# Kernel optimization log

Measured on AMD Instinct MI355X. Metric: run time of the kernel, lower is better.

Reference implementation:

```python
import jax, jax.numpy as jnp
import numpy as np

B, T, D_IN, D_OUT = 4, 2048, 1024, 1024

def setup_inputs() -> dict:
    key = jax.random.key(0)
    k0, k1, k2, k3 = jax.random.split(key, 4)
    s = 1.0 / np.sqrt(D_IN)
    return {
        "x": jax.random.normal(k0, (B, T, D_IN), dtype=jnp.float32),
        "w_query": jax.random.normal(k1, (D_OUT, D_IN), dtype=jnp.float32) * s,
        "w_key": jax.random.normal(k2, (D_OUT, D_IN), dtype=jnp.float32) * s,
        "w_value": jax.random.normal(k3, (D_OUT, D_IN), dtype=jnp.float32) * s,
    }

def reference(x, w_query, w_key, w_value):
    # Linear (no bias): y = x @ W.T, W has shape (d_out, d_in)
    q = jnp.einsum('btd,od->bto', x, w_query)   # (B,T,d_out)
    k = jnp.einsum('btd,od->bto', x, w_key)
    v = jnp.einsum('btd,od->bto', x, w_value)
    scale = 1.0 / jnp.sqrt(jnp.asarray(k.shape[-1], dtype=x.dtype))
    scores = jnp.einsum('bqo,bko->bqk', q, k) * scale  # (B,T,T)
    t = scores.shape[-1]
    causal = jnp.tril(jnp.ones((t, t), dtype=bool))    # True = keep
    scores = jnp.where(causal, scores, -jnp.inf)
    weights = jax.nn.softmax(scores, axis=-1)
    # dropout rate is 0.0 -> identity
    context = jnp.einsum('bqk,bko->bqo', weights, v)   # (B,T,d_out)
    return context
```

## Files before the change

kernel.cpp:

```cpp
#include <hip/hip_runtime.h>
#include <hip/hip_bf16.h>

#define NB 4
#define TT 2048
#define DD 1024
#define MM (NB*TT)

using f32x4  = __attribute__((ext_vector_type(4))) float;
using bf16x8 = __attribute__((ext_vector_type(8))) __bf16;
using u16x8  = __attribute__((ext_vector_type(8))) unsigned short;

__device__ __forceinline__ unsigned short f2b(float f) {
  __hip_bfloat16 h = __float2bfloat16(f);
  return *reinterpret_cast<unsigned short*>(&h);
}

__device__ __forceinline__ float b2f(unsigned short u) {
  __hip_bfloat16 h = *reinterpret_cast<__hip_bfloat16*>(&u);
  return __bfloat162float(h);
}

__device__ __forceinline__ void gld_lds16(const void* g, void* l) {
  __builtin_amdgcn_global_load_lds(
      (const __attribute__((address_space(1))) void*)g,
      (__attribute__((address_space(3))) void*)l, 16, 0, 0);
}

__device__ __forceinline__ void bar() {
  asm volatile("" ::: "memory");
  __builtin_amdgcn_s_barrier();
  asm volatile("" ::: "memory");
}

__global__ void k_cvt4(const float* __restrict__ x,  const float* __restrict__ wq,
                       const float* __restrict__ wk, const float* __restrict__ wv,
                       unsigned short* __restrict__ xb, unsigned short* __restrict__ wqb,
                       unsigned short* __restrict__ wkb, unsigned short* __restrict__ wvb) {
  const int nx = MM*DD/4, nw = DD*DD/4;
  const int ntot = nx + 3*nw;
  int i = blockIdx.x * blockDim.x + threadIdx.x;
  int stride = gridDim.x * blockDim.x;
  for (; i < ntot; i += stride) {
    const float* s; unsigned short* d; int j;
    if (i < nx)            { s = x;  d = xb;  j = i; }
    else if (i < nx + nw)  { s = wq; d = wqb; j = i - nx; }
    else if (i < nx + 2*nw){ s = wk; d = wkb; j = i - nx - nw; }
    else                   { s = wv; d = wvb; j = i - nx - 2*nw; }
    float4 v = reinterpret_cast<const float4*>(s)[j];
    ushort4 o;
    o.x = f2b(v.x); o.y = f2b(v.y); o.z = f2b(v.z); o.w = f2b(v.w);
    reinterpret_cast<ushort4*>(d)[j] = o;
  }
}

__launch_bounds__(512, 2)
__global__ void k_qkv8(const unsigned short* __restrict__ xb,
                       const unsigned short* __restrict__ wqb,
                       const unsigned short* __restrict__ wkb,
                       const unsigned short* __restrict__ wvb,
                       unsigned short* __restrict__ Qb,
                       unsigned short* __restrict__ Kb,
                       unsigned short* __restrict__ Vt) {
  __shared__ __align__(16) char Lds[131072];
  const int tid = threadIdx.x;
  const int l = tid & 63, wid = tid >> 6;
  const int l15 = l & 15, l4 = l >> 4;
  const int wm = wid >> 2, wn = wid & 3;
  const int z = blockIdx.z;
  const unsigned short* W = (z == 0) ? wqb : (z == 1) ? wkb : wvb;
  const size_t m0 = (size_t)blockIdx.x * 256;
  const size_t n0 = (size_t)blockIdx.y * 256;

  int srow[2], scb[2];
  #pragma unroll
  for (int j = 0; j < 2; ++j) {
    int d  = (j*512 + tid) * 16;
    int sd = d ^ (((d >> 7) & 7) << 4);
    srow[j] = sd >> 7;
    scb[j]  = sd & 127;
  }
  const char* pA[2][2]; const char* pB[2][2];
  #pragma unroll
  for (int h = 0; h < 2; ++h)
    #pragma unroll
    for (int j = 0; j < 2; ++j) {
      pA[h][j] = (const char*)xb + ((m0 + h*128 + srow[j]) * DD) * 2 + scb[j];
      pB[h][j] = (const char*)W  + ((n0 + h*128 + srow[j]) * DD) * 2 + scb[j];
    }
  char* ldsA = Lds;
  char* ldsB = Lds + 65536;

#define STG(p, ldsr, slot, half, kt) do {                                         \
    gld_lds16(p[half][0] + (size_t)(kt)*128,                                      \
              (ldsr) + (slot)*32768 + (half)*16384 + wid*1024);                   \
    gld_lds16(p[half][1] + (size_t)(kt)*128,                                      \
              (ldsr) + (slot)*32768 + (half)*16384 + 8192 + wid*1024);            \
  } while (0)

#define SWZ(x) ((x) ^ ((((x) >> 7) & 7) << 4))
#define KTQ 16
  STG(pA, ldsA, 0, 0, 0);
  STG(pA, ldsA, 0, 1, 0);
  STG(pB, ldsB, 0, 0, 0);
  STG(pB, ldsB, 0, 1, 0);
  STG(pA, ldsA, 1, 0, 1);
  STG(pA, ldsA, 1, 1, 1);
  STG(pB, ldsB, 1, 0, 1);
  asm volatile("s_waitcnt vmcnt(6)" ::: "memory");
  bar();

  f32x4 acc[8][4] = {};
  bf16x8 afL[4][2], afU[4][2], bfL[2][2], bfR[2][2];

#define TILE(t, S) do {                                                           \
    const int tn = ((t)+1 < KTQ) ? (t)+1 : 0;                                     \
    const int t2 = ((t)+2 < KTQ) ? (t)+2 : 0;                                     \
           \
    _Pragma("unroll") for (int m = 0; m < 4; ++m)                                 \
      _Pragma("unroll") for (int kk = 0; kk < 2; ++kk) {                          \
        int lg = m*2048 + l15*128 + kk*64 + l4*16;                                \
        afL[m][kk] = *(const bf16x8*)(ldsA + (S)*32768 + wm*16384 + SWZ(lg)); }   \
    _Pragma("unroll") for (int n = 0; n < 2; ++n)                                 \
      _Pragma("unroll") for (int kk = 0; kk < 2; ++kk) {                          \
        int lg = ((wn&1)*64 + n*16 + l15)*128 + kk*64 + l4*16;                    \
        bfL[n][kk] = *(const bf16x8*)(ldsB + (S)*32768 + (wn>>1)*16384 + SWZ(lg)); } \
    STG(pB, ldsB, (S)^1, 1, tn);                                                  \
    bar();                                                                        \
    asm volatile("s_waitcnt lgkmcnt(0)" ::: "memory");                            \
    __builtin_amdgcn_sched_barrier(0);                                            \
    __builtin_amdgcn_s_setprio(1);                                                \
    _Pragma("unroll") for (int m = 0; m < 4; ++m)                                 \
      _Pragma("unroll") for (int n = 0; n < 2; ++n)                               \
        _Pragma("unroll") for (int kk = 0; kk < 2; ++kk)                          \
          acc[m][n] = __builtin_amdgcn_mfma_f32_16x16x32_bf16(afL[m][kk], bfL[n][kk], acc[m][n], 0,0,0); \
    __builtin_amdgcn_s_setprio(0);                                                \
    bar();                                                                        \
                                    \
    _Pragma("unroll") for (int m = 0; m < 4; ++m)                                 \
      _Pragma("unroll") for (int kk = 0; kk < 2; ++kk) {                          \
        int lg = (m+4)*2048 + l15*128 + kk*64 + l4*16;                            \
        afU[m][kk] = *(const bf16x8*)(ldsA + (S)*32768 + wm*16384 + SWZ(lg)); }   \
    bar();                                                                        \
    asm volatile("s_waitcnt lgkmcnt(0)" ::: "memory");                            \
    __builtin_amdgcn_sched_barrier(0);                                            \
    __builtin_amdgcn_s_setprio(1);                                                \
    _Pragma("unroll") for (int m = 0; m < 4; ++m)                                 \
      _Pragma("unroll") for (int n = 0; n < 2; ++n)                               \
        _Pragma("unroll") for (int kk = 0; kk < 2; ++kk)                          \
          acc[m+4][n] = __builtin_amdgcn_mfma_f32_16x16x32_bf16(afU[m][kk], bfL[n][kk], acc[m+4][n], 0,0,0); \
    __builtin_amdgcn_s_setprio(0);                                                \
    bar();                                                                        \
                    \
    _Pragma("unroll") for (int n = 0; n < 2; ++n)                                 \
      _Pragma("unroll") for (int kk = 0; kk < 2; ++kk) {                          \
        int lg = ((wn&1)*64 + (n+2)*16 + l15)*128 + kk*64 + l4*16;                \
        bfR[n][kk] = *(const bf16x8*)(ldsB + (S)*32768 + (wn>>1)*16384 + SWZ(lg)); } \
    STG(pA, ldsA, S, 0, t2);                                                      \
    bar();                                                                        \
    asm volatile("s_waitcnt lgkmcnt(0)" ::: "memory");                            \
    __builtin_amdgcn_sched_barrier(0);                                            \
    __builtin_amdgcn_s_setprio(1);                                                \
    _Pragma("unroll") for (int m = 0; m < 4; ++m)                                 \
      _Pragma("unroll") for (int n = 0; n < 2; ++n)                               \
        _Pragma("unroll") for (int kk = 0; kk < 2; ++kk)                          \
          acc[m+4][n+2] = __builtin_amdgcn_mfma_f32_16x16x32_bf16(afU[m][kk], bfR[n][kk], acc[m+4][n+2], 0,0,0); \
    __builtin_amdgcn_s_setprio(0);                                                \
    bar();                                                                        \
              \
    STG(pA, ldsA, S, 1, t2);                                                      \
    STG(pB, ldsB, S, 0, t2);                                                      \
    asm volatile("s_waitcnt vmcnt(6)" ::: "memory");                              \
    bar();                                                                        \
    __builtin_amdgcn_s_setprio(1);                                                \
    _Pragma("unroll") for (int m = 0; m < 4; ++m)                                 \
      _Pragma("unroll") for (int n = 0; n < 2; ++n)                               \
        _Pragma("unroll") for (int kk = 0; kk < 2; ++kk)                          \
          acc[m][n+2] = __builtin_amdgcn_mfma_f32_16x16x32_bf16(afL[m][kk], bfR[n][kk], acc[m][n+2], 0,0,0); \
    __builtin_amdgcn_s_setprio(0);                                                \
    bar();                                                                        \
  } while (0)

  for (int tp = 0; tp < KTQ; tp += 2) {
    TILE(tp, 0);
    TILE(tp + 1, 1);
  }
#undef TILE
#undef STG
#undef SWZ
  asm volatile("s_waitcnt vmcnt(0)" ::: "memory");

  if (z < 2) {
    unsigned short* out = (z == 0) ? Qb : Kb;
    #pragma unroll
    for (int m = 0; m < 8; ++m)
      #pragma unroll
      for (int n = 0; n < 4; ++n)
        #pragma unroll
        for (int r = 0; r < 4; ++r) {
          size_t row = m0 + wm*128 + m*16 + l4*4 + r;
          size_t col = n0 + wn*64  + n*16 + l15;
          out[row * DD + col] = f2b(acc[m][n][r]);
        }
  } else {
    #pragma unroll
    for (int m = 0; m < 8; ++m)
      #pragma unroll
      for (int n = 0; n < 4; ++n)
        #pragma unroll
        for (int r = 0; r < 4; ++r) {
          size_t row = m0 + wm*128 + m*16 + l4*4 + r;
          size_t col = n0 + wn*64  + n*16 + l15;
          size_t b = row >> 11, t = row & (TT - 1);
          Vt[(b * DD + col) * TT + t] = f2b(acc[m][n][r]);
        }
  }
}

__launch_bounds__(256)
__global__ void k_scores(const unsigned short* __restrict__ Qb,
                         const unsigned short* __restrict__ Kb,
                         unsigned short* __restrict__ S) {
  __shared__ __align__(16) unsigned short As[128*32];
  __shared__ __align__(16) unsigned short Bs[128*32];
  const int tid = threadIdx.x;
  const int l = tid & 63, wid = tid >> 6;
  const int l15 = l & 15, l4 = l >> 4;
  const int wr = (wid >> 1) * 64, wc = (wid & 1) * 64;

  const int b = blockIdx.x / 136;
  int t = blockIdx.x % 136;
  int qi = 0;
  while ((qi + 1) * (qi + 2) / 2 <= t) qi++;
  const int ki = t - qi * (qi + 1) / 2;

  const size_t arow0 = (size_t)b * TT + qi * 128;
  const size_t brow0 = (size_t)b * TT + ki * 128;

  const int lrow = tid >> 2;
  const int lcol = (tid & 3) * 8;
  const unsigned short* Ap = Qb + (arow0 + lrow) * DD + lcol;
  const unsigned short* Bp = Kb + (brow0 + lrow) * DD + lcol;
  unsigned short* AsW = &As[wid * 512];
  unsigned short* BsW = &Bs[wid * 512];

  f32x4 acc[4][4] = {};

  for (int k0 = 0; k0 < DD; k0 += 32) {
    __syncthreads();
    gld_lds16(Ap + k0,           AsW);
    gld_lds16(Ap + 64*DD + k0,   AsW + 2048);
    gld_lds16(Bp + k0,           BsW);
    gld_lds16(Bp + 64*DD + k0,   BsW + 2048);
    __syncthreads();
    bf16x8 af[4], bfr[4];
    #pragma unroll
    for (int mi = 0; mi < 4; ++mi)
      af[mi] = *reinterpret_cast<const bf16x8*>(&As[(wr + mi*16 + l15)*32 + l4*8]);
    #pragma unroll
    for (int ni = 0; ni < 4; ++ni)
      bfr[ni] = *reinterpret_cast<const bf16x8*>(&Bs[(wc + ni*16 + l15)*32 + l4*8]);
    #pragma unroll
    for (int mi = 0; mi < 4; ++mi)
      #pragma unroll
      for (int ni = 0; ni < 4; ++ni)
        acc[mi][ni] = __builtin_amdgcn_mfma_f32_16x16x32_bf16(af[mi], bfr[ni], acc[mi][ni], 0, 0, 0);
  }

  const float scale = 0.03125f;
  #pragma unroll
  for (int mi = 0; mi < 4; ++mi)
    #pragma unroll
    for (int ni = 0; ni < 4; ++ni)
      #pragma unroll
      for (int r = 0; r < 4; ++r) {
        int row = wr + mi*16 + l4*4 + r;
        int col = wc + ni*16 + l15;
        int gq = qi*128 + row, gk = ki*128 + col;
        float v = (gk > gq) ? -1e30f : acc[mi][ni][r] * scale;
        S[((size_t)b * TT + gq) * TT + gk] = f2b(v);
      }
}

__launch_bounds__(256)
__global__ void k_softmax(unsigned short* __restrict__ S, float* __restrict__ rl) {
  const int tid = threadIdx.x;
  const int w = tid >> 6, l = tid & 63;
  const int row = blockIdx.x * 4 + w;
  const int b = row >> 11, q = row & (TT - 1);
  unsigned short* Srow = S + ((size_t)b * TT + q) * TT;
  const int width = ((q >> 7) + 1) << 7;

  float v[4][8];
  bool has[4];
  float mx = -1e30f;
  #pragma unroll
  for (int c = 0; c < 4; ++c) {
    const int off = c * 512 + l * 8;
    has[c] = off < width;
    if (has[c]) {
      u16x8 u = *reinterpret_cast<const u16x8*>(&Srow[off]);
      #pragma unroll
      for (int j = 0; j < 8; ++j) { v[c][j] = b2f(u[j]); mx = fmaxf(mx, v[c][j]); }
    }
  }
  #pragma unroll
  for (int mm = 1; mm < 64; mm <<= 1) mx = fmaxf(mx, __shfl_xor(mx, mm));

  float s = 0.f;
  #pragma unroll
  for (int c = 0; c < 4; ++c) {
    if (has[c]) {
      u16x8 u;
      #pragma unroll
      for (int j = 0; j < 8; ++j) {
        float p = __expf(v[c][j] - mx);
        s += p;
        u[j] = f2b(p);
      }
      *reinterpret_cast<u16x8*>(&Srow[c * 512 + l * 8]) = u;
    }
  }
  #pragma unroll
  for (int mm = 1; mm < 64; mm <<= 1) s += __shfl_xor(s, mm);
  if (l == 0) rl[row] = 1.0f / s;
}

__launch_bounds__(256)
__global__ void k_pv(const unsigned short* __restrict__ P,
                     const unsigned short* __restrict__ Vt,
                     const float* __restrict__ rl,
                     float* __restrict__ O) {
  __shared__ __align__(16) unsigned short As[128*32];
  __shared__ __align__(16) unsigned short Bs[128*32];
  const int tid = threadIdx.x;
  const int l = tid & 63, wid = tid >> 6;
  const int l15 = l & 15, l4 = l >> 4;
  const int wr = (wid >> 1) * 64, wc = (wid & 1) * 64;

  const int qi = 15 - (blockIdx.x >> 5);
  const int di = (blockIdx.x >> 2) & 7;
  const int b  = blockIdx.x & 3;
  const int KEXT = (qi + 1) * 128;

  const int lrow = tid >> 2;
  const int lcol = (tid & 3) * 8;
  const unsigned short* Ap = P  + ((size_t)b * TT + qi * 128 + lrow) * TT + lcol;
  const unsigned short* Bp = Vt + ((size_t)b * DD + di * 128 + lrow) * TT + lcol;
  unsigned short* AsW = &As[wid * 512];
  unsigned short* BsW = &Bs[wid * 512];

  f32x4 acc[4][4] = {};

  for (int k0 = 0; k0 < KEXT; k0 += 32) {
    __syncthreads();
    gld_lds16(Ap + k0,           AsW);
    gld_lds16(Ap + 64*TT + k0,   AsW + 2048);
    gld_lds16(Bp + k0,           BsW);
    gld_lds16(Bp + 64*TT + k0,   BsW + 2048);
    __syncthreads();
    bf16x8 af[4], bfr[4];
    #pragma unroll
    for (int mi = 0; mi < 4; ++mi)
      af[mi] = *reinterpret_cast<const bf16x8*>(&As[(wr + mi*16 + l15)*32 + l4*8]);
    #pragma unroll
    for (int ni = 0; ni < 4; ++ni)
      bfr[ni] = *reinterpret_cast<const bf16x8*>(&Bs[(wc + ni*16 + l15)*32 + l4*8]);
    #pragma unroll
    for (int mi = 0; mi < 4; ++mi)
      #pragma unroll
      for (int ni = 0; ni < 4; ++ni)
        acc[mi][ni] = __builtin_amdgcn_mfma_f32_16x16x32_bf16(af[mi], bfr[ni], acc[mi][ni], 0, 0, 0);
  }

  #pragma unroll
  for (int mi = 0; mi < 4; ++mi)
    #pragma unroll
    for (int ni = 0; ni < 4; ++ni)
      #pragma unroll
      for (int r = 0; r < 4; ++r) {
        int row = wr + mi*16 + l4*4 + r;
        int col = wc + ni*16 + l15;
        size_t q = (size_t)qi * 128 + row;
        O[((size_t)b * TT + q) * DD + di * 128 + col] =
            acc[mi][ni][r] * rl[(size_t)b * TT + q];
      }
}

extern "C" void kernel_launch(void* const* d_in, const int* in_sizes, int n_in,
                              void* d_out, int out_size, void* d_ws, size_t ws_size,
                              hipStream_t stream) {
  const float* x  = (const float*)d_in[0];
  const float* wq = (const float*)d_in[1];
  const float* wk = (const float*)d_in[2];
  const float* wv = (const float*)d_in[3];
  unsigned short* ws  = (unsigned short*)d_ws;
  unsigned short* Qb  = ws;
  unsigned short* Kb  = Qb + (size_t)MM * DD;
  unsigned short* Vt  = Kb + (size_t)MM * DD;
  unsigned short* Sb  = Vt + (size_t)MM * DD;
  unsigned short* xb  = Sb;
  unsigned short* wqb = xb + (size_t)MM * DD;
  unsigned short* wkb = wqb + (size_t)DD * DD;
  unsigned short* wvb = wkb + (size_t)DD * DD;
  float* rl = (float*)(Sb + (size_t)NB * TT * TT);
  float* out = (float*)d_out;

  k_cvt4<<<2048, 256, 0, stream>>>(x, wq, wk, wv, xb, wqb, wkb, wvb);
  k_qkv8<<<dim3(32, 4, 3), 512, 0, stream>>>(xb, wqb, wkb, wvb, Qb, Kb, Vt);
  k_scores<<<544, 256, 0, stream>>>(Qb, Kb, Sb);
  k_softmax<<<MM/4, 256, 0, stream>>>(Sb, rl);
  k_pv<<<512, 256, 0, stream>>>(Sb, Vt, rl, out);
}
```

Measured before the change: 188.5 us.

## Double K-step to 64 with XOR-swizzled LDS in scores and PV kernels

In the scores and PV GEMM kernels, the K step per iteration doubles from 32 to 64, so each barrier pair covers twice as much MFMA work. Global-to-LDS loads use an XOR-swizzled column mapping that matches a swizzled LDS read pattern, meant to avoid LDS bank conflicts with the wider 128-byte rows. The scores kernel also remaps block indices so concurrently scheduled blocks spread across batches and tiles. LDS use per block doubles, and the projection kernel edits are only reformatting of index arithmetic.

```diff
diff --git a/kernel.cpp b/kernel.cpp
--- a/kernel.cpp
+++ b/kernel.cpp
@@ -115,14 +115,14 @@
 #define TILE(t, S) do {                                                           \
     const int tn = ((t)+1 < KTQ) ? (t)+1 : 0;                                     \
     const int t2 = ((t)+2 < KTQ) ? (t)+2 : 0;                                     \
-           \
+      \
     _Pragma("unroll") for (int m = 0; m < 4; ++m)                                 \
       _Pragma("unroll") for (int kk = 0; kk < 2; ++kk) {                          \
-        int lg = m*2048 + l15*128 + kk*64 + l4*16;                                \
+        int lg = (m*16 + l15)*128 + (kk*64 + l4*16);                              \
         afL[m][kk] = *(const bf16x8*)(ldsA + (S)*32768 + wm*16384 + SWZ(lg)); }   \
     _Pragma("unroll") for (int n = 0; n < 2; ++n)                                 \
       _Pragma("unroll") for (int kk = 0; kk < 2; ++kk) {                          \
-        int lg = ((wn&1)*64 + n*16 + l15)*128 + kk*64 + l4*16;                    \
+        int lg = ((wn&1)*64 + n*16 + l15)*128 + (kk*64 + l4*16);                  \
         bfL[n][kk] = *(const bf16x8*)(ldsB + (S)*32768 + (wn>>1)*16384 + SWZ(lg)); } \
     STG(pB, ldsB, (S)^1, 1, tn);                                                  \
     bar();                                                                        \
@@ -135,10 +135,10 @@
           acc[m][n] = __builtin_amdgcn_mfma_f32_16x16x32_bf16(afL[m][kk], bfL[n][kk], acc[m][n], 0,0,0); \
     __builtin_amdgcn_s_setprio(0);                                                \
     bar();                                                                        \
-                                    \
+                        \
     _Pragma("unroll") for (int m = 0; m < 4; ++m)                                 \
       _Pragma("unroll") for (int kk = 0; kk < 2; ++kk) {                          \
-        int lg = (m+4)*2048 + l15*128 + kk*64 + l4*16;                            \
+        int lg = ((m+4)*16 + l15)*128 + (kk*64 + l4*16);                          \
         afU[m][kk] = *(const bf16x8*)(ldsA + (S)*32768 + wm*16384 + SWZ(lg)); }   \
     bar();                                                                        \
     asm volatile("s_waitcnt lgkmcnt(0)" ::: "memory");                            \
@@ -150,10 +150,10 @@
           acc[m+4][n] = __builtin_amdgcn_mfma_f32_16x16x32_bf16(afU[m][kk], bfL[n][kk], acc[m+4][n], 0,0,0); \
     __builtin_amdgcn_s_setprio(0);                                                \
     bar();                                                                        \
-                    \
+               \
     _Pragma("unroll") for (int n = 0; n < 2; ++n)                                 \
       _Pragma("unroll") for (int kk = 0; kk < 2; ++kk) {                          \
-        int lg = ((wn&1)*64 + (n+2)*16 + l15)*128 + kk*64 + l4*16;                \
+        int lg = ((wn&1)*64 + (n+2)*16 + l15)*128 + (kk*64 + l4*16);              \
         bfR[n][kk] = *(const bf16x8*)(ldsB + (S)*32768 + (wn>>1)*16384 + SWZ(lg)); } \
     STG(pA, ldsA, S, 0, t2);                                                      \
     bar();                                                                        \
@@ -166,7 +166,7 @@
           acc[m+4][n+2] = __builtin_amdgcn_mfma_f32_16x16x32_bf16(afU[m][kk], bfR[n][kk], acc[m+4][n+2], 0,0,0); \
     __builtin_amdgcn_s_setprio(0);                                                \
     bar();                                                                        \
-              \
+        \
     STG(pA, ldsA, S, 1, t2);                                                      \
     STG(pB, ldsB, S, 0, t2);                                                      \
     asm volatile("s_waitcnt vmcnt(6)" ::: "memory");                              \
@@ -220,15 +220,17 @@
 __global__ void k_scores(const unsigned short* __restrict__ Qb,
                          const unsigned short* __restrict__ Kb,
                          unsigned short* __restrict__ S) {
-  __shared__ __align__(16) unsigned short As[128*32];
-  __shared__ __align__(16) unsigned short Bs[128*32];
+  __shared__ __align__(16) unsigned short As[128*64];
+  __shared__ __align__(16) unsigned short Bs[128*64];
   const int tid = threadIdx.x;
   const int l = tid & 63, wid = tid >> 6;
   const int l15 = l & 15, l4 = l >> 4;
   const int wr = (wid >> 1) * 64, wc = (wid & 1) * 64;
 
-  const int b = blockIdx.x / 136;
-  int t = blockIdx.x % 136;
+  const int bid = blockIdx.x;
+  const int swz = (bid & 7) * 68 + (bid >> 3);
+  const int b = swz / 136;
+  int t = swz % 136;
   int qi = 0;
   while ((qi + 1) * (qi + 2) / 2 <= t) qi++;
   const int ki = t - qi * (qi + 1) / 2;
@@ -236,34 +238,44 @@
   const size_t arow0 = (size_t)b * TT + qi * 128;
   const size_t brow0 = (size_t)b * TT + ki * 128;
 
-  const int lrow = tid >> 2;
-  const int lcol = (tid & 3) * 8;
-  const unsigned short* Ap = Qb + (arow0 + lrow) * DD + lcol;
-  const unsigned short* Bp = Kb + (brow0 + lrow) * DD + lcol;
+  const int srow = wid * 8 + (l >> 3);
+  const int scol = 8 * ((l & 7) ^ (l >> 3));
+  const unsigned short* Ap = Qb + (arow0 + srow) * DD + scol;
+  const unsigned short* Bp = Kb + (brow0 + srow) * DD + scol;
   unsigned short* AsW = &As[wid * 512];
   unsigned short* BsW = &Bs[wid * 512];
 
   f32x4 acc[4][4] = {};
 
-  for (int k0 = 0; k0 < DD; k0 += 32) {
+  for (int k0 = 0; k0 < DD; k0 += 64) {
     __syncthreads();
-    gld_lds16(Ap + k0,           AsW);
-    gld_lds16(Ap + 64*DD + k0,   AsW + 2048);
-    gld_lds16(Bp + k0,           BsW);
-    gld_lds16(Bp + 64*DD + k0,   BsW + 2048);
+    #pragma unroll
+    for (int u = 0; u < 4; ++u) {
+      gld_lds16(Ap + (size_t)u*32*DD + k0, AsW + u*2048);
+      gld_lds16(Bp + (size_t)u*32*DD + k0, BsW + u*2048);
+    }
     __syncthreads();
-    bf16x8 af[4], bfr[4];
-    #pragma unroll
-    for (int mi = 0; mi < 4; ++mi)
-      af[mi] = *reinterpret_cast<const bf16x8*>(&As[(wr + mi*16 + l15)*32 + l4*8]);
-    #pragma unroll
-    for (int ni = 0; ni < 4; ++ni)
-      bfr[ni] = *reinterpret_cast<const bf16x8*>(&Bs[(wc + ni*16 + l15)*32 + l4*8]);
-    #pragma unroll
-    for (int mi = 0; mi < 4; ++mi)
-      #pragma unroll
-      for (int ni = 0; ni < 4; ++ni)
-        acc[mi][ni] = __builtin_amdgcn_mfma_f32_16x16x32_bf16(af[mi], bfr[ni], acc[mi][ni], 0, 0, 0);
+    #pragma unroll
+    for (int kk = 0; kk < 2; ++kk) {
+      bf16x8 af[4], bfr[4];
+      #pragma unroll
+      for (int mi = 0; mi < 4; ++mi) {
+        int ro = wr + mi*16 + l15;
+        int off = ro*128 + ((kk*64 + l4*16) ^ ((ro & 7) << 4));
+        af[mi] = *reinterpret_cast<const bf16x8*>((const char*)As + off);
+      }
+      #pragma unroll
+      for (int ni = 0; ni < 4; ++ni) {
+        int ro = wc + ni*16 + l15;
+        int off = ro*128 + ((kk*64 + l4*16) ^ ((ro & 7) << 4));
+        bfr[ni] = *reinterpret_cast<const bf16x8*>((const char*)Bs + off);
+      }
+      #pragma unroll
+      for (int mi = 0; mi < 4; ++mi)
+        #pragma unroll
+        for (int ni = 0; ni < 4; ++ni)
+          acc[mi][ni] = __builtin_amdgcn_mfma_f32_16x16x32_bf16(af[mi], bfr[ni], acc[mi][ni], 0, 0, 0);
+    }
   }
 
   const float scale = 0.03125f;
@@ -330,8 +342,8 @@
                      const unsigned short* __restrict__ Vt,
                      const float* __restrict__ rl,
                      float* __restrict__ O) {
-  __shared__ __align__(16) unsigned short As[128*32];
-  __shared__ __align__(16) unsigned short Bs[128*32];
+  __shared__ __align__(16) unsigned short As[128*64];
+  __shared__ __align__(16) unsigned short Bs[128*64];
   const int tid = threadIdx.x;
   const int l = tid & 63, wid = tid >> 6;
   const int l15 = l & 15, l4 = l >> 4;
@@ -342,34 +354,44 @@
   const int b  = blockIdx.x & 3;
   const int KEXT = (qi + 1) * 128;
 
-  const int lrow = tid >> 2;
-  const int lcol = (tid & 3) * 8;
-  const unsigned short* Ap = P  + ((size_t)b * TT + qi * 128 + lrow) * TT + lcol;
-  const unsigned short* Bp = Vt + ((size_t)b * DD + di * 128 + lrow) * TT + lcol;
+  const int srow = wid * 8 + (l >> 3);
+  const int scol = 8 * ((l & 7) ^ (l >> 3));
+  const unsigned short* Ap = P  + ((size_t)b * TT + qi * 128 + srow) * TT + scol;
+  const unsigned short* Bp = Vt + ((size_t)b * DD + di * 128 + srow) * TT + scol;
   unsigned short* AsW = &As[wid * 512];
   unsigned short* BsW = &Bs[wid * 512];
 
   f32x4 acc[4][4] = {};
 
-  for (int k0 = 0; k0 < KEXT; k0 += 32) {
+  for (int k0 = 0; k0 < KEXT; k0 += 64) {
     __syncthreads();
-    gld_lds16(Ap + k0,           AsW);
-    gld_lds16(Ap + 64*TT + k0,   AsW + 2048);
-    gld_lds16(Bp + k0,           BsW);
-    gld_lds16(Bp + 64*TT + k0,   BsW + 2048);
+    #pragma unroll
+    for (int u = 0; u < 4; ++u) {
+      gld_lds16(Ap + (size_t)u*32*TT + k0, AsW + u*2048);
+      gld_lds16(Bp + (size_t)u*32*TT + k0, BsW + u*2048);
+    }
     __syncthreads();
-    bf16x8 af[4], bfr[4];
-    #pragma unroll
-    for (int mi = 0; mi < 4; ++mi)
-      af[mi] = *reinterpret_cast<const bf16x8*>(&As[(wr + mi*16 + l15)*32 + l4*8]);
-    #pragma unroll
-    for (int ni = 0; ni < 4; ++ni)
-      bfr[ni] = *reinterpret_cast<const bf16x8*>(&Bs[(wc + ni*16 + l15)*32 + l4*8]);
-    #pragma unroll
-    for (int mi = 0; mi < 4; ++mi)
-      #pragma unroll
-      for (int ni = 0; ni < 4; ++ni)
-        acc[mi][ni] = __builtin_amdgcn_mfma_f32_16x16x32_bf16(af[mi], bfr[ni], acc[mi][ni], 0, 0, 0);
+    #pragma unroll
+    for (int kk = 0; kk < 2; ++kk) {
+      bf16x8 af[4], bfr[4];
+      #pragma unroll
+      for (int mi = 0; mi < 4; ++mi) {
+        int ro = wr + mi*16 + l15;
+        int off = ro*128 + ((kk*64 + l4*16) ^ ((ro & 7) << 4));
+        af[mi] = *reinterpret_cast<const bf16x8*>((const char*)As + off);
+      }
+      #pragma unroll
+      for (int ni = 0; ni < 4; ++ni) {
+        int ro = wc + ni*16 + l15;
+        int off = ro*128 + ((kk*64 + l4*16) ^ ((ro & 7) << 4));
+        bfr[ni] = *reinterpret_cast<const bf16x8*>((const char*)Bs + off);
+      }
+      #pragma unroll
+      for (int mi = 0; mi < 4; ++mi)
+        #pragma unroll
+        for (int ni = 0; ni < 4; ++ni)
+          acc[mi][ni] = __builtin_amdgcn_mfma_f32_16x16x32_bf16(af[mi], bfr[ni], acc[mi][ni], 0, 0, 0);
+    }
   }
 
   #pragma unroll
```

New measurement: 177.5 us. 1.06x faster.
